# Kernel tuning notes

Measured on AMD Instinct MI355X. Metric: run time of the kernel, lower is better.

## Reference

```python
import math
import jax, jax.numpy as jnp
import numpy as np

HIDDEN = 1024
HEADS = 16
HEAD_DIM = HIDDEN // HEADS
PRIME = 7
MAX_ITERS = 10
ENT_THRESH = 0.2
PRIME_SCALE = 1.0 / math.sqrt(PRIME * HEAD_DIM)
EPS = 1e-6


def setup_inputs() -> dict:
    key = jax.random.key(0)
    ks = jax.random.split(key, 6)
    B, S = 2, 2048
    w = 0.02
    return {
        "hidden_states": jax.random.normal(ks[0], (B, S, HIDDEN), jnp.float32),
        "q_w": jax.random.normal(ks[1], (HIDDEN, HIDDEN), jnp.float32) * w,
        "q_b": jnp.zeros((HIDDEN,), jnp.float32),
        "k_w": jax.random.normal(ks[2], (HIDDEN, HIDDEN), jnp.float32) * w,
        "k_b": jnp.zeros((HIDDEN,), jnp.float32),
        "v_w": jax.random.normal(ks[3], (HIDDEN, HIDDEN), jnp.float32) * w,
        "v_b": jnp.zeros((HIDDEN,), jnp.float32),
        "o_w": jax.random.normal(ks[4], (HIDDEN, HIDDEN), jnp.float32) * w,
        "o_b": jnp.zeros((HIDDEN,), jnp.float32),
        "attention_mask": jnp.ones((B, S), jnp.int32),
    }


def _split_heads(x):
    B, S, _ = x.shape
    return x.reshape(B, S, HEADS, HEAD_DIM).transpose(0, 2, 1, 3)


def reference(hidden_states, q_w, q_b, k_w, k_b, v_w, v_b, o_w, o_b, attention_mask):
    B, S, _ = hidden_states.shape
    # projections (torch Linear: x @ W^T + b)
    q = _split_heads(hidden_states @ q_w.T + q_b) * PRIME_SCALE  # [B,H,S,hd]
    k = _split_heads(hidden_states @ k_w.T + k_b)
    v = _split_heads(hidden_states @ v_w.T + v_b)

    scores = jnp.einsum("bhqd,bhkd->bhqk", q, k)  # [B,H,S,S]
    mask = attention_mask[:, None, None, :]
    scores = jnp.where(mask == 0, -jnp.inf, scores)
    attn = jax.nn.softmax(scores, axis=-1)  # dropout p=0 (eval)

    base = jnp.einsum("bhqk,bhkd->bhqd", attn, v)  # attention_weights @ v

    # entropy of the (fixed) attention weights: [B,H]
    entropy = -jnp.sum(attn * jnp.log(attn + EPS), axis=-1).mean(axis=-1)
    avg_entropy = entropy.mean()

    # loop never changes attn, so entropy is constant: either break at i=1 or run all
    full = base
    for i in range(1, MAX_ITERS):
        blend = 1.0 / (1.0 + math.exp(-i / MAX_ITERS))          # sigmoid(i/max)
        res_scale = 0.5 + 0.5 * blend                            # resonance scale
        full = (1.0 - blend) * full + blend * (res_scale * base)

    out_heads = jnp.where(avg_entropy < ENT_THRESH, base, full)  # [B,H,S,hd]

    merged = out_heads.transpose(0, 2, 1, 3).reshape(B, S, HIDDEN)
    return merged @ o_w.T + o_b
```

## Files before the change

kernel.cpp:

```cpp
#include <hip/hip_runtime.h>
#include <hip/hip_bf16.h>
#include <stdint.h>


#define PRIME_SCALE 0.047245559126654356f
#define LOG2E       1.4426950408889634f
#define LN2         0.6931471805599453f
#define QSCALE      (PRIME_SCALE * LOG2E)
#define BLEND_C     0.85096556f

#if __has_builtin(__builtin_amdgcn_exp2f)
#define EXP2(x) __builtin_amdgcn_exp2f(x)
#else
#define EXP2(x) exp2f(x)
#endif

typedef __attribute__((ext_vector_type(8))) short short8;
typedef __attribute__((ext_vector_type(4))) float f32x4;

__device__ __forceinline__ unsigned short f2bf(float x) {
    union { float f; unsigned int u; } v; v.f = x;
    unsigned int r = (v.u + 0x7fffu + ((v.u >> 16) & 1u)) >> 16;
    return (unsigned short)r;
}
__device__ __forceinline__ unsigned short f2bf_fast(float x) {
    union { float f; unsigned int u; } v; v.f = x;
    return (unsigned short)((v.u + 0x8000u) >> 16);
}
__device__ __forceinline__ float bf2f(unsigned short x) {
    union { unsigned int u; float f; } v; v.u = ((unsigned int)x) << 16;
    return v.f;
}
__device__ __forceinline__ unsigned cvtpk_bf16(float lo, float hi) {
    unsigned r;
    asm("v_cvt_pk_bf16_f32 %0, %1, %2" : "=v"(r) : "v"(lo), "v"(hi));
    return r;
}

__device__ __forceinline__ void glds16(const unsigned short* g, unsigned short* l) {
    __builtin_amdgcn_global_load_lds((const __attribute__((address_space(1))) unsigned int*)g,
                                     (__attribute__((address_space(3))) unsigned int*)l,
                                     16, 0, 0);
}

__global__ void zero_out_f32(float* p, int n) {
    int i = blockIdx.x * 256 + threadIdx.x;
    if (i < n) p[i] = 0.f;
}

__global__ __launch_bounds__(256) void cvt5(
    const float* __restrict__ s0, const float* __restrict__ s1, const float* __restrict__ s2,
    const float* __restrict__ s3, const float* __restrict__ s4,
    unsigned short* __restrict__ d0, unsigned short* __restrict__ d1, unsigned short* __restrict__ d2,
    unsigned short* __restrict__ d3, unsigned short* __restrict__ d4, float* entp)
{
    if (blockIdx.x == 0 && threadIdx.x == 0) entp[0] = 0.f;
    unsigned int i = blockIdx.x * 256 + threadIdx.x;
    const float* s; unsigned short* d; unsigned int off;
    if (i < (1u << 20)) { s = s0; d = d0; off = i; }
    else {
        unsigned int j = i - (1u << 20);
        unsigned int sel = j >> 18; off = j & 0x3FFFFu;
        s = sel == 0 ? s1 : sel == 1 ? s2 : sel == 2 ? s3 : s4;
        d = sel == 0 ? d1 : sel == 1 ? d2 : sel == 2 ? d3 : d4;
    }
    float4 v = ((const float4*)s)[off];
    ushort4 p; p.x = f2bf(v.x); p.y = f2bf(v.y); p.z = f2bf(v.z); p.w = f2bf(v.w);
    ((ushort4*)d)[off] = p;
}

__global__ __launch_bounds__(256) void gemm_qkv(
    const unsigned short* __restrict__ hsb,
    const unsigned short* __restrict__ qwb, const unsigned short* __restrict__ kwb,
    const unsigned short* __restrict__ vwb,
    const float* __restrict__ qb, const float* __restrict__ kb, const float* __restrict__ vb,
    unsigned short* __restrict__ Qo, unsigned short* __restrict__ Ko, unsigned short* __restrict__ Vto)
{
    const int bid = blockIdx.x;
    const int op = bid >> 8, local = bid & 255;
    const unsigned short *A, *B; const float* bias; unsigned short* C;
    int m0, n0, ldc, biasRow; float scale;
    if (op == 0)      { A = hsb; B = qwb; bias = qb; C = Qo;  m0 = (local >> 3) * 128; n0 = (local & 7) * 128;  ldc = 1024; biasRow = 0; scale = QSCALE; }
    else if (op == 1) { A = hsb; B = kwb; bias = kb; C = Ko;  m0 = (local >> 3) * 128; n0 = (local & 7) * 128;  ldc = 1024; biasRow = 0; scale = 1.f; }
    else              { A = vwb; B = hsb; bias = vb; C = Vto; m0 = (local >> 5) * 128; n0 = (local & 31) * 128; ldc = 4096; biasRow = 1; scale = 1.f; }

    __shared__ unsigned short As[128 * 32];
    __shared__ unsigned short Bs[128 * 32];
    const int t = threadIdx.x, lane = t & 63, w = t >> 6;
    const int quad = lane >> 4, l15 = lane & 15;
    const int wr = (w >> 1) * 64, wc = (w & 1) * 64;
    const int srow = lane >> 2, scol = (lane & 3) * 8;

    f32x4 acc[4][4];
#pragma unroll
    for (int i = 0; i < 4; ++i)
#pragma unroll
        for (int j = 0; j < 4; ++j) acc[i][j] = (f32x4){0.f, 0.f, 0.f, 0.f};

    for (int kk = 0; kk < 32; ++kk) {
        const int k0 = kk * 32;
#pragma unroll
        for (int j = 0; j < 2; ++j) {
            int row = (w * 2 + j) * 16 + srow;
            glds16(&A[(size_t)(m0 + row) * 1024 + k0 + scol], &As[(w * 2 + j) * 512]);
            glds16(&B[(size_t)(n0 + row) * 1024 + k0 + scol], &Bs[(w * 2 + j) * 512]);
        }
        __syncthreads();
        short8 af[4], bf[4];
#pragma unroll
        for (int mt = 0; mt < 4; ++mt) af[mt] = *(const short8*)&As[(wr + mt * 16 + l15) * 32 + quad * 8];
#pragma unroll
        for (int nt = 0; nt < 4; ++nt) bf[nt] = *(const short8*)&Bs[(wc + nt * 16 + l15) * 32 + quad * 8];
#pragma unroll
        for (int mt = 0; mt < 4; ++mt)
#pragma unroll
            for (int nt = 0; nt < 4; ++nt)
                acc[mt][nt] = __builtin_amdgcn_mfma_f32_16x16x32_bf16(af[mt], bf[nt], acc[mt][nt], 0, 0, 0);
        __syncthreads();
    }
#pragma unroll
    for (int mt = 0; mt < 4; ++mt) {
#pragma unroll
        for (int nt = 0; nt < 4; ++nt) {
            int n = n0 + wc + nt * 16 + l15;
#pragma unroll
            for (int r = 0; r < 4; ++r) {
                int m = m0 + wr + mt * 16 + quad * 4 + r;
                float bval = biasRow ? bias[m] : bias[n];
                C[(size_t)m * ldc + n] = f2bf((acc[mt][nt][r] + bval) * scale);
            }
        }
    }
}

__global__ __launch_bounds__(256, 3) void flash_split(
    const unsigned short* __restrict__ Q,
    const unsigned short* __restrict__ K,
    const unsigned short* __restrict__ Vt,
    const int* __restrict__ mask,
    unsigned short* __restrict__ O0, unsigned short* __restrict__ O1,
    float* __restrict__ lpart, float* __restrict__ Tpart)
{
    const int qt = blockIdx.x;
    const int bh = blockIdx.y;
    const int z  = blockIdx.z;
    const int b = bh >> 4, h = bh & 15;
    const int t = threadIdx.x, lane = t & 63, w = t >> 6;
    const int quad = lane >> 4, l15 = lane & 15;
    const int r8 = lane >> 3, ch8 = lane & 7;
    const int kt0 = z * 16, kt1 = kt0 + 16;
    unsigned short* __restrict__ Opart = z ? O1 : O0;

    __shared__ unsigned short Qs[128 * 72];
    __shared__ unsigned short Ks[2][64 * 64];
    __shared__ unsigned short Vs[2][64 * 64];
    __shared__ unsigned int maskBits[64];

    const int* maskb = mask + b * 2048;
    {
        const int4* mp = (const int4*)(maskb + t * 8);
        int4 a = mp[0], c = mp[1];
        unsigned bits = (unsigned)(a.x != 0)       | ((unsigned)(a.y != 0) << 1)
                      | ((unsigned)(a.z != 0) << 2) | ((unsigned)(a.w != 0) << 3)
                      | ((unsigned)(c.x != 0) << 4) | ((unsigned)(c.y != 0) << 5)
                      | ((unsigned)(c.z != 0) << 6) | ((unsigned)(c.w != 0) << 7);
        ((unsigned char*)maskBits)[t] = (unsigned char)bits;
    }
    {
        const int row0 = w * 16;
#pragma unroll
        for (int i = 0; i < 2; ++i) {
            int row = row0 + i * 8 + r8;
            int c = ch8 ^ (row & 7);
            glds16(&K[(size_t)(b * 2048 + kt0 * 64 + row) * 1024 + h * 64 + c * 8], &Ks[0][(row0 + i * 8) * 64]);
            glds16(&Vt[(size_t)(h * 64 + row) * 4096 + b * 2048 + kt0 * 64 + c * 8], &Vs[0][(row0 + i * 8) * 64]);
        }
    }
#pragma unroll
    for (int i = 0; i < 4; ++i) {
        int f = i * 256 + t; int row = f >> 3, c = f & 7;
        uint4 v = *(const uint4*)&Q[(size_t)(b * 2048 + qt * 128 + row) * 1024 + h * 64 + c * 8];
        *(uint4*)&Qs[row * 72 + c * 8] = v;
    }
    __syncthreads();

    short8 qa[2][2];
#pragma unroll
    for (int st = 0; st < 2; ++st) {
        int qrow = w * 32 + st * 16 + l15;
        qa[st][0] = *(const short8*)&Qs[qrow * 72 + quad * 8];
        qa[st][1] = *(const short8*)&Qs[qrow * 72 + 32 + quad * 8];
    }
    unsigned short* Ps = Qs;

    float l_r[2] = {0.f, 0.f}, T_r[2] = {0.f, 0.f};
    f32x4 o_acc[2][4];
#pragma unroll
    for (int st = 0; st < 2; ++st)
#pragma unroll
        for (int nt = 0; nt < 4; ++nt) o_acc[st][nt] = (f32x4){0.f, 0.f, 0.f, 0.f};

    for (int kt = kt0; kt < kt1; ++kt) {
        const int cur = kt & 1;
        if (kt < kt1 - 1) {
            const int kn = (kt + 1) * 64;
            const int row0 = w * 16;
#pragma unroll
            for (int i = 0; i < 2; ++i) {
                int row = row0 + i * 8 + r8;
                int c = ch8 ^ (row & 7);
                glds16(&K[(size_t)(b * 2048 + kn + row) * 1024 + h * 64 + c * 8], &Ks[cur ^ 1][(row0 + i * 8) * 64]);
                glds16(&Vt[(size_t)(h * 64 + row) * 4096 + b * 2048 + kn + c * 8], &Vs[cur ^ 1][(row0 + i * 8) * 64]);
            }
        }

        f32x4 sacc[4][2];
#pragma unroll
        for (int nt = 0; nt < 4; ++nt)
#pragma unroll
            for (int st = 0; st < 2; ++st) sacc[nt][st] = (f32x4){0.f, 0.f, 0.f, 0.f};
        __builtin_amdgcn_s_setprio(1);
#pragma unroll
        for (int nt = 0; nt < 4; ++nt) {
            int krow = nt * 16 + l15;
            short8 kf0 = *(const short8*)&Ks[cur][krow * 64 + ((quad ^ (krow & 7)) * 8)];
            short8 kf1 = *(const short8*)&Ks[cur][krow * 64 + (((quad + 4) ^ (krow & 7)) * 8)];
#pragma unroll
            for (int st = 0; st < 2; ++st) {
                sacc[nt][st] = __builtin_amdgcn_mfma_f32_16x16x32_bf16(kf0, qa[st][0], sacc[nt][st], 0, 0, 0);
                sacc[nt][st] = __builtin_amdgcn_mfma_f32_16x16x32_bf16(kf1, qa[st][1], sacc[nt][st], 0, 0, 0);
            }
        }
        __builtin_amdgcn_s_setprio(0);

        unsigned mwA = maskBits[kt * 2], mwB = maskBits[kt * 2 + 1];
#pragma unroll
        for (int nt = 0; nt < 4; ++nt) {
            unsigned mw = (nt & 2) ? mwB : mwA;
            unsigned mb = (mw >> (((nt & 1) << 4) + (quad << 2))) & 0xFu;
#pragma unroll
            for (int st = 0; st < 2; ++st) {
                float s0 = (mb & 1u) ? sacc[nt][st][0] : -1.0e30f;
                float s1 = (mb & 2u) ? sacc[nt][st][1] : -1.0e30f;
                float s2 = (mb & 4u) ? sacc[nt][st][2] : -1.0e30f;
                float s3 = (mb & 8u) ? sacc[nt][st][3] : -1.0e30f;
                float p0 = EXP2(s0), p1 = EXP2(s1), p2 = EXP2(s2), p3 = EXP2(s3);
                l_r[st] += (p0 + p1) + (p2 + p3);
                T_r[st] += (p0 * s0 + p1 * s1) + (p2 * s2 + p3 * s3);
                uint2 pk;
                pk.x = cvtpk_bf16(p0, p1);
                pk.y = cvtpk_bf16(p2, p3);
                *(uint2*)&Ps[(w * 32 + st * 16 + l15) * 72 + nt * 16 + quad * 4] = pk;
            }
        }

#pragma unroll
        for (int ks = 0; ks < 2; ++ks) {
            short8 pa[2];
#pragma unroll
            for (int st = 0; st < 2; ++st)
                pa[st] = *(const short8*)&Ps[(w * 32 + st * 16 + l15) * 72 + ks * 32 + quad * 8];
            __builtin_amdgcn_s_setprio(1);
#pragma unroll
            for (int nt = 0; nt < 4; ++nt) {
                int vrow = nt * 16 + l15;
                short8 vf = *(const short8*)&Vs[cur][vrow * 64 + ((((ks * 4 + quad)) ^ (vrow & 7)) * 8)];
#pragma unroll
                for (int st = 0; st < 2; ++st)
                    o_acc[st][nt] = __builtin_amdgcn_mfma_f32_16x16x32_bf16(pa[st], vf, o_acc[st][nt], 0, 0, 0);
            }
            __builtin_amdgcn_s_setprio(0);
        }
        __syncthreads();
    }

#pragma unroll
    for (int st = 0; st < 2; ++st) {
        float l = l_r[st], T = T_r[st];
        l += __shfl_xor(l, 16); T += __shfl_xor(T, 16);
        l += __shfl_xor(l, 32); T += __shfl_xor(T, 32);
        if (lane < 16) {
            int qrow = qt * 128 + w * 32 + st * 16 + l15;
            int li = z * 65536 + bh * 2048 + qrow;
            lpart[li] = l; Tpart[li] = T;
        }
#pragma unroll
        for (int r = 0; r < 4; ++r) {
            int mrow = b * 2048 + qt * 128 + w * 32 + st * 16 + quad * 4 + r;
#pragma unroll
            for (int nt = 0; nt < 4; ++nt)
                Opart[(size_t)mrow * 1024 + h * 64 + nt * 16 + l15] = f2bf_fast(o_acc[st][nt][r]);
        }
    }
}

__global__ __launch_bounds__(256) void combine_split(
    unsigned short* __restrict__ O0, const unsigned short* __restrict__ O1,
    const float* __restrict__ lpart)
{
    unsigned idx = blockIdx.x * 256 + threadIdx.x;
    int mrow = idx >> 8;
    int c4 = (idx & 255) << 2;
    int h = c4 >> 6;
    int b = mrow >> 11, qrow = mrow & 2047;
    int li = (b * 16 + h) * 2048 + qrow;
    float l = lpart[li] + lpart[65536 + li];
    float inv = 1.0f / l;

    ushort4 a = ((const ushort4*)O0)[idx];
    ushort4 c = ((const ushort4*)O1)[idx];
    ushort4 o;
    o.x = f2bf_fast((bf2f(a.x) + bf2f(c.x)) * inv);
    o.y = f2bf_fast((bf2f(a.y) + bf2f(c.y)) * inv);
    o.z = f2bf_fast((bf2f(a.z) + bf2f(c.z)) * inv);
    o.w = f2bf_fast((bf2f(a.w) + bf2f(c.w)) * inv);
    ((ushort4*)O0)[idx] = o;
}

__global__ __launch_bounds__(256) void entropy_k(
    const float* __restrict__ lpart, const float* __restrict__ Tpart,
    float* __restrict__ entp)
{
    __shared__ float wsum[4];
    int idx = blockIdx.x * 256 + threadIdx.x;
    float acc = 0.f;
#pragma unroll
    for (int i = 0; i < 4; ++i) {
        int r = idx * 4 + i;
        float l = lpart[r] + lpart[65536 + r];
        float T = Tpart[r] + Tpart[65536 + r];
        acc += __log2f(l) - T / l;
    }
    acc += __shfl_xor(acc, 1);
    acc += __shfl_xor(acc, 2);
    acc += __shfl_xor(acc, 4);
    acc += __shfl_xor(acc, 8);
    acc += __shfl_xor(acc, 16);
    acc += __shfl_xor(acc, 32);
    int lane = threadIdx.x & 63, w = threadIdx.x >> 6;
    if (lane == 0) wsum[w] = acc;
    __syncthreads();
    if (threadIdx.x == 0)
        atomicAdd(entp, LN2 * (wsum[0] + wsum[1] + wsum[2] + wsum[3]));
}

__global__ __launch_bounds__(256) void gemm_out_bf(
    const unsigned short* __restrict__ A, const unsigned short* __restrict__ Bw,
    const float* __restrict__ bias, const float* __restrict__ entp,
    float* __restrict__ C)
{
    const float avg = entp[0] * (1.0f / 65536.0f);
    const float scale = (avg < 0.2f) ? 1.0f : BLEND_C;

    const int m0 = blockIdx.x * 128;
    const int n0 = blockIdx.y * 64;
    __shared__ unsigned short As[128 * 32];
    __shared__ unsigned short Bs[64 * 32];
    const int t = threadIdx.x, lane = t & 63, w = t >> 6;
    const int quad = lane >> 4, l15 = lane & 15;
    const int wr = (w >> 1) * 64, wc = (w & 1) * 32;
    const int srow = lane >> 2, scol = (lane & 3) * 8;

    f32x4 acc[4][2];
#pragma unroll
    for (int i = 0; i < 4; ++i)
#pragma unroll
        for (int j = 0; j < 2; ++j) acc[i][j] = (f32x4){0.f, 0.f, 0.f, 0.f};

    for (int kk = 0; kk < 32; ++kk) {
        const int k0 = kk * 32;
#pragma unroll
        for (int j = 0; j < 2; ++j) {
            int row = (w * 2 + j) * 16 + srow;
            glds16(&A[(size_t)(m0 + row) * 1024 + k0 + scol], &As[(w * 2 + j) * 512]);
        }
        {
            int row = w * 16 + srow;
            glds16(&Bw[(size_t)(n0 + row) * 1024 + k0 + scol], &Bs[w * 512]);
        }
        __syncthreads();
        short8 af[4], bf[2];
#pragma unroll
        for (int mt = 0; mt < 4; ++mt) af[mt] = *(const short8*)&As[(wr + mt * 16 + l15) * 32 + quad * 8];
#pragma unroll
        for (int nt = 0; nt < 2; ++nt) bf[nt] = *(const short8*)&Bs[(wc + nt * 16 + l15) * 32 + quad * 8];
#pragma unroll
        for (int mt = 0; mt < 4; ++mt)
#pragma unroll
            for (int nt = 0; nt < 2; ++nt)
                acc[mt][nt] = __builtin_amdgcn_mfma_f32_16x16x32_bf16(af[mt], bf[nt], acc[mt][nt], 0, 0, 0);
        __syncthreads();
    }
#pragma unroll
    for (int mt = 0; mt < 4; ++mt) {
#pragma unroll
        for (int nt = 0; nt < 2; ++nt) {
            int n = n0 + wc + nt * 16 + l15;
#pragma unroll
            for (int r = 0; r < 4; ++r) {
                int m = m0 + wr + mt * 16 + quad * 4 + r;
                C[(size_t)m * 1024 + n] = scale * acc[mt][nt][r] + bias[n];
            }
        }
    }
}

extern "C" void kernel_launch(void* const* d_in, const int* in_sizes, int n_in,
                              void* d_out, int out_size, void* d_ws, size_t ws_size,
                              hipStream_t stream)
{
    const float* hs = (const float*)d_in[0];
    const float* qw = (const float*)d_in[1];
    const float* qb = (const float*)d_in[2];
    const float* kw = (const float*)d_in[3];
    const float* kb = (const float*)d_in[4];
    const float* vw = (const float*)d_in[5];
    const float* vb = (const float*)d_in[6];
    const float* ow = (const float*)d_in[7];
    const float* ob = (const float*)d_in[8];
    const int*   mask = (const int*)d_in[9];
    float* out = (float*)d_out;

    const size_t MB = 1024 * 1024;
    char* ws = (char*)d_ws;
    dim3 blk(256);

    if (ws_size >= 50 * MB) {
        unsigned short* hsb = (unsigned short*)(ws);
        unsigned short* Q   = (unsigned short*)(ws + 8 * MB);
        unsigned short* Kp  = (unsigned short*)(ws + 16 * MB);
        unsigned short* Vt  = (unsigned short*)(ws + 24 * MB);
        unsigned short* qwb = (unsigned short*)(ws + 32 * MB);
        unsigned short* kwb = (unsigned short*)(ws + 34 * MB);
        unsigned short* vwb = (unsigned short*)(ws + 36 * MB);
        unsigned short* owb = (unsigned short*)(ws + 38 * MB);
        float* entp         = (float*)(ws + 40 * MB);
        unsigned short* Op1 = (unsigned short*)(ws + 41 * MB);
        float* lpart        = (float*)(ws + 49 * MB);
        float* Tpart        = (float*)(ws + 49 * MB + 524288);
        unsigned short* Op0 = hsb;

        cvt5<<<dim3(8192), blk, 0, stream>>>(hs, qw, kw, vw, ow, hsb, qwb, kwb, vwb, owb, entp);
        gemm_qkv<<<dim3(768), blk, 0, stream>>>(hsb, qwb, kwb, vwb, qb, kb, vb, Q, Kp, Vt);
        flash_split<<<dim3(16, 32, 2), blk, 0, stream>>>(Q, Kp, Vt, mask, Op0, Op1, lpart, Tpart);
        combine_split<<<dim3(4096), blk, 0, stream>>>(Op0, Op1, lpart);
        entropy_k<<<dim3(64), blk, 0, stream>>>(lpart, Tpart, entp);
        gemm_out_bf<<<dim3(32, 16), blk, 0, stream>>>(Op0, owb, ob, entp, out);
    } else {
        zero_out_f32<<<dim3((out_size + 255) / 256), blk, 0, stream>>>(out, out_size);
    }
}
```

Baseline: 211.5 us.

## Double flash query tile to 256 rows and load mask per tile via ballot

Each flash block now handles 256 query rows instead of 128, with 64 rows per wave, so every K/V tile loaded into shared memory is reused across twice as many queries. The grid is halved and launch bounds drop to 2 blocks per SM to make room for the extra registers. Q and P shared storage moves to an XOR-swizzled 64-wide layout instead of padding. The shared mask bitmap is replaced by a per-tile global load plus a wave ballot. Fewer blocks (512) and higher register pressure may reduce occupancy and latency hiding.

```diff
diff --git a/kernel.cpp b/kernel.cpp
--- a/kernel.cpp
+++ b/kernel.cpp
@@ -133,7 +133,7 @@
     }
 }
 
-__global__ __launch_bounds__(256, 3) void flash_split(
+__global__ __launch_bounds__(256, 2) void flash_split(
     const unsigned short* __restrict__ Q,
     const unsigned short* __restrict__ K,
     const unsigned short* __restrict__ Vt,
@@ -151,21 +151,12 @@
     const int kt0 = z * 16, kt1 = kt0 + 16;
     unsigned short* __restrict__ Opart = z ? O1 : O0;
 
-    __shared__ unsigned short Qs[128 * 72];
+    __shared__ unsigned short Qs[256 * 64];
     __shared__ unsigned short Ks[2][64 * 64];
     __shared__ unsigned short Vs[2][64 * 64];
-    __shared__ unsigned int maskBits[64];
 
     const int* maskb = mask + b * 2048;
-    {
-        const int4* mp = (const int4*)(maskb + t * 8);
-        int4 a = mp[0], c = mp[1];
-        unsigned bits = (unsigned)(a.x != 0)       | ((unsigned)(a.y != 0) << 1)
-                      | ((unsigned)(a.z != 0) << 2) | ((unsigned)(a.w != 0) << 3)
-                      | ((unsigned)(c.x != 0) << 4) | ((unsigned)(c.y != 0) << 5)
-                      | ((unsigned)(c.z != 0) << 6) | ((unsigned)(c.w != 0) << 7);
-        ((unsigned char*)maskBits)[t] = (unsigned char)bits;
-    }
+
     {
         const int row0 = w * 16;
 #pragma unroll
@@ -177,31 +168,44 @@
         }
     }
 #pragma unroll
-    for (int i = 0; i < 4; ++i) {
+    for (int i = 0; i < 8; ++i) {
         int f = i * 256 + t; int row = f >> 3, c = f & 7;
-        uint4 v = *(const uint4*)&Q[(size_t)(b * 2048 + qt * 128 + row) * 1024 + h * 64 + c * 8];
-        *(uint4*)&Qs[row * 72 + c * 8] = v;
+        uint4 v = *(const uint4*)&Q[(size_t)(b * 2048 + qt * 256 + row) * 1024 + h * 64 + c * 8];
+        int rx = row & 15;
+        uint2 plo; plo.x = v.x; plo.y = v.y;
+        uint2 phi; phi.x = v.z; phi.y = v.w;
+        *(uint2*)&Qs[row * 64 + (((2 * c) ^ rx) << 2)]     = plo;
+        *(uint2*)&Qs[row * 64 + (((2 * c + 1) ^ rx) << 2)] = phi;
     }
     __syncthreads();
 
-    short8 qa[2][2];
-#pragma unroll
-    for (int st = 0; st < 2; ++st) {
-        int qrow = w * 32 + st * 16 + l15;
-        qa[st][0] = *(const short8*)&Qs[qrow * 72 + quad * 8];
-        qa[st][1] = *(const short8*)&Qs[qrow * 72 + 32 + quad * 8];
+    short8 qa[4][2];
+#pragma unroll
+    for (int st = 0; st < 4; ++st) {
+        int prow = (w * 64 + st * 16 + l15) * 64;
+#pragma unroll
+        for (int hf = 0; hf < 2; ++hf) {
+            int p0 = hf * 8 + quad * 2;
+            union { uint2 u2[2]; short8 s8; } uu;
+            uu.u2[0] = *(const uint2*)&Qs[prow + ((p0 ^ l15) << 2)];
+            uu.u2[1] = *(const uint2*)&Qs[prow + (((p0 + 1) ^ l15) << 2)];
+            qa[st][hf] = uu.s8;
+        }
     }
     unsigned short* Ps = Qs;
 
-    float l_r[2] = {0.f, 0.f}, T_r[2] = {0.f, 0.f};
-    f32x4 o_acc[2][4];
-#pragma unroll
-    for (int st = 0; st < 2; ++st)
+    float l_r[4] = {0.f, 0.f, 0.f, 0.f}, T_r[4] = {0.f, 0.f, 0.f, 0.f};
+    f32x4 o_acc[4][4];
+#pragma unroll
+    for (int st = 0; st < 4; ++st)
 #pragma unroll
         for (int nt = 0; nt < 4; ++nt) o_acc[st][nt] = (f32x4){0.f, 0.f, 0.f, 0.f};
+
+    int mv = maskb[kt0 * 64 + lane];
 
     for (int kt = kt0; kt < kt1; ++kt) {
         const int cur = kt & 1;
+        int mv_next = 0;
         if (kt < kt1 - 1) {
             const int kn = (kt + 1) * 64;
             const int row0 = w * 16;
@@ -212,81 +216,82 @@
                 glds16(&K[(size_t)(b * 2048 + kn + row) * 1024 + h * 64 + c * 8], &Ks[cur ^ 1][(row0 + i * 8) * 64]);
                 glds16(&Vt[(size_t)(h * 64 + row) * 4096 + b * 2048 + kn + c * 8], &Vs[cur ^ 1][(row0 + i * 8) * 64]);
             }
-        }
-
-        f32x4 sacc[4][2];
-#pragma unroll
-        for (int nt = 0; nt < 4; ++nt)
-#pragma unroll
-            for (int st = 0; st < 2; ++st) sacc[nt][st] = (f32x4){0.f, 0.f, 0.f, 0.f};
-        __builtin_amdgcn_s_setprio(1);
+            mv_next = maskb[kn + 64 + lane - 64];
+        }
+        unsigned long long bal = __ballot(mv != 0);
+        unsigned mwA = (unsigned)bal, mwB = (unsigned)(bal >> 32);
+
 #pragma unroll
         for (int nt = 0; nt < 4; ++nt) {
             int krow = nt * 16 + l15;
             short8 kf0 = *(const short8*)&Ks[cur][krow * 64 + ((quad ^ (krow & 7)) * 8)];
             short8 kf1 = *(const short8*)&Ks[cur][krow * 64 + (((quad + 4) ^ (krow & 7)) * 8)];
-#pragma unroll
-            for (int st = 0; st < 2; ++st) {
-                sacc[nt][st] = __builtin_amdgcn_mfma_f32_16x16x32_bf16(kf0, qa[st][0], sacc[nt][st], 0, 0, 0);
-                sacc[nt][st] = __builtin_amdgcn_mfma_f32_16x16x32_bf16(kf1, qa[st][1], sacc[nt][st], 0, 0, 0);
-            }
-        }
-        __builtin_amdgcn_s_setprio(0);
-
-        unsigned mwA = maskBits[kt * 2], mwB = maskBits[kt * 2 + 1];
-#pragma unroll
-        for (int nt = 0; nt < 4; ++nt) {
+            f32x4 sv[4];
+            __builtin_amdgcn_s_setprio(1);
+#pragma unroll
+            for (int st = 0; st < 4; ++st) {
+                sv[st] = __builtin_amdgcn_mfma_f32_16x16x32_bf16(kf0, qa[st][0], (f32x4){0.f, 0.f, 0.f, 0.f}, 0, 0, 0);
+                sv[st] = __builtin_amdgcn_mfma_f32_16x16x32_bf16(kf1, qa[st][1], sv[st], 0, 0, 0);
+            }
+            __builtin_amdgcn_s_setprio(0);
             unsigned mw = (nt & 2) ? mwB : mwA;
             unsigned mb = (mw >> (((nt & 1) << 4) + (quad << 2))) & 0xFu;
 #pragma unroll
-            for (int st = 0; st < 2; ++st) {
-                float s0 = (mb & 1u) ? sacc[nt][st][0] : -1.0e30f;
-                float s1 = (mb & 2u) ? sacc[nt][st][1] : -1.0e30f;
-                float s2 = (mb & 4u) ? sacc[nt][st][2] : -1.0e30f;
-                float s3 = (mb & 8u) ? sacc[nt][st][3] : -1.0e30f;
+            for (int st = 0; st < 4; ++st) {
+                float s0 = (mb & 1u) ? sv[st][0] : -1.0e30f;
+                float s1 = (mb & 2u) ? sv[st][1] : -1.0e30f;
+                float s2 = (mb & 4u) ? sv[st][2] : -1.0e30f;
+                float s3 = (mb & 8u) ? sv[st][3] : -1.0e30f;
                 float p0 = EXP2(s0), p1 = EXP2(s1), p2 = EXP2(s2), p3 = EXP2(s3);
                 l_r[st] += (p0 + p1) + (p2 + p3);
                 T_r[st] += (p0 * s0 + p1 * s1) + (p2 * s2 + p3 * s3);
                 uint2 pk;
                 pk.x = cvtpk_bf16(p0, p1);
                 pk.y = cvtpk_bf16(p2, p3);
-                *(uint2*)&Ps[(w * 32 + st * 16 + l15) * 72 + nt * 16 + quad * 4] = pk;
+                *(uint2*)&Ps[(w * 64 + st * 16 + l15) * 64 + (((nt * 4 + quad) ^ l15) << 2)] = pk;
             }
         }
 
 #pragma unroll
         for (int ks = 0; ks < 2; ++ks) {
-            short8 pa[2];
-#pragma unroll
-            for (int st = 0; st < 2; ++st)
-                pa[st] = *(const short8*)&Ps[(w * 32 + st * 16 + l15) * 72 + ks * 32 + quad * 8];
+            short8 pa[4];
+#pragma unroll
+            for (int st = 0; st < 4; ++st) {
+                int prow = (w * 64 + st * 16 + l15) * 64;
+                int p0 = ks * 8 + quad * 2;
+                union { uint2 u2[2]; short8 s8; } uu;
+                uu.u2[0] = *(const uint2*)&Ps[prow + ((p0 ^ l15) << 2)];
+                uu.u2[1] = *(const uint2*)&Ps[prow + (((p0 + 1) ^ l15) << 2)];
+                pa[st] = uu.s8;
+            }
             __builtin_amdgcn_s_setprio(1);
 #pragma unroll
             for (int nt = 0; nt < 4; ++nt) {
                 int vrow = nt * 16 + l15;
                 short8 vf = *(const short8*)&Vs[cur][vrow * 64 + ((((ks * 4 + quad)) ^ (vrow & 7)) * 8)];
 #pragma unroll
-                for (int st = 0; st < 2; ++st)
+                for (int st = 0; st < 4; ++st)
                     o_acc[st][nt] = __builtin_amdgcn_mfma_f32_16x16x32_bf16(pa[st], vf, o_acc[st][nt], 0, 0, 0);
             }
             __builtin_amdgcn_s_setprio(0);
         }
         __syncthreads();
-    }
-
-#pragma unroll
-    for (int st = 0; st < 2; ++st) {
+        mv = mv_next;
+    }
+
+#pragma unroll
+    for (int st = 0; st < 4; ++st) {
         float l = l_r[st], T = T_r[st];
         l += __shfl_xor(l, 16); T += __shfl_xor(T, 16);
         l += __shfl_xor(l, 32); T += __shfl_xor(T, 32);
         if (lane < 16) {
-            int qrow = qt * 128 + w * 32 + st * 16 + l15;
+            int qrow = qt * 256 + w * 64 + st * 16 + l15;
             int li = z * 65536 + bh * 2048 + qrow;
             lpart[li] = l; Tpart[li] = T;
         }
 #pragma unroll
         for (int r = 0; r < 4; ++r) {
-            int mrow = b * 2048 + qt * 128 + w * 32 + st * 16 + quad * 4 + r;
+            int mrow = b * 2048 + qt * 256 + w * 64 + st * 16 + quad * 4 + r;
 #pragma unroll
             for (int nt = 0; nt < 4; ++nt)
                 Opart[(size_t)mrow * 1024 + h * 64 + nt * 16 + l15] = f2bf_fast(o_acc[st][nt][r]);
@@ -442,7 +447,7 @@
 
         cvt5<<<dim3(8192), blk, 0, stream>>>(hs, qw, kw, vw, ow, hsb, qwb, kwb, vwb, owb, entp);
         gemm_qkv<<<dim3(768), blk, 0, stream>>>(hsb, qwb, kwb, vwb, qb, kb, vb, Q, Kp, Vt);
-        flash_split<<<dim3(16, 32, 2), blk, 0, stream>>>(Q, Kp, Vt, mask, Op0, Op1, lpart, Tpart);
+        flash_split<<<dim3(8, 32, 2), blk, 0, stream>>>(Q, Kp, Vt, mask, Op0, Op1, lpart, Tpart);
         combine_split<<<dim3(4096), blk, 0, stream>>>(Op0, Op1, lpart);
         entropy_k<<<dim3(64), blk, 0, stream>>>(lpart, Tpart, entp);
         gemm_out_bf<<<dim3(32, 16), blk, 0, stream>>>(Op0, owb, ob, entp, out);
```

Result: faster. 204.4 us (-3.4%).
